# Performance work log

Hardware: AMD Instinct MI355X
Metric: run time of the kernel (lower is better)

Reference implementation:

```python
import jax, jax.numpy as jnp
import numpy as np
from jax.scipy.linalg import expm

HIDDEN = 1024
STATE = 64
INTER = 4096
EPS = 1e-06
DT_MIN, DT_MAX = 0.001, 0.1


def rmsnorm(x, w, eps=EPS):
    var = jnp.mean(x * x, axis=-1, keepdims=True)
    return x * jax.lax.rsqrt(var + eps) * w


def setup_inputs() -> dict:
    key = jax.random.key(0)
    ks = jax.random.split(key, 10)
    hidden_states = jax.random.normal(ks[0], (4, 2048, HIDDEN), dtype=jnp.float32)
    A = jax.random.normal(ks[1], (STATE, STATE), dtype=jnp.float32) * 0.01
    B = jax.random.normal(ks[2], (STATE, HIDDEN), dtype=jnp.float32) * 0.01
    C = jax.random.normal(ks[3], (HIDDEN, STATE), dtype=jnp.float32) * 0.01
    D = jnp.ones((HIDDEN,), dtype=jnp.float32)
    log_dt = jax.random.uniform(ks[4], (HIDDEN,), dtype=jnp.float32) * (np.log(DT_MAX) - np.log(DT_MIN)) + np.log(DT_MIN)
    s = 1.0 / np.sqrt(HIDDEN)
    w_gate = jax.random.uniform(ks[5], (INTER, HIDDEN), minval=-s, maxval=s, dtype=jnp.float32)
    w_up = jax.random.uniform(ks[6], (INTER, HIDDEN), minval=-s, maxval=s, dtype=jnp.float32)
    s2 = 1.0 / np.sqrt(INTER)
    w_down = jax.random.uniform(ks[7], (HIDDEN, INTER), minval=-s2, maxval=s2, dtype=jnp.float32)
    ln1_w = jnp.ones((HIDDEN,), dtype=jnp.float32)
    ln2_w = jnp.ones((HIDDEN,), dtype=jnp.float32)
    return {"hidden_states": hidden_states, "A": A, "B": B, "C": C, "D": D,
            "log_dt": log_dt, "w_gate": w_gate, "w_up": w_up, "w_down": w_down,
            "ln1_w": ln1_w, "ln2_w": ln2_w}


def ssm(x, A, B, C, D, log_dt):
    # x: (batch, seq, hidden)
    dt = jnp.exp(log_dt)                    # (hidden,)
    A_bar = expm(A * jnp.mean(dt))          # (state, state)
    B_bar = B * dt[None, :]                 # (state, hidden)

    def step(state, x_t):
        # state: (batch, state); x_t: (batch, hidden)
        state = state @ A_bar.T + x_t @ B_bar.T
        out = state @ C.T + D * x_t
        return state, out

    x_t = jnp.swapaxes(x, 0, 1)             # (seq, batch, hidden)
    init = jnp.zeros((x.shape[0], A.shape[0]), dtype=x.dtype)
    _, ys = jax.lax.scan(step, init, x_t)
    return jnp.swapaxes(ys, 0, 1)           # (batch, seq, hidden)


def reference(hidden_states, A, B, C, D, log_dt, w_gate, w_up, w_down, ln1_w, ln2_w):
    # pre-norm SSM mixer + residual
    residual = hidden_states
    h = rmsnorm(hidden_states, ln1_w)
    h = ssm(h, A, B, C, D, log_dt)
    h = residual + h
    # pre-norm SwiGLU FFN + residual
    residual = h
    hn = rmsnorm(h, ln2_w)
    gate = hn @ w_gate.T
    up = hn @ w_up.T
    ffn = (jax.nn.silu(gate) * up) @ w_down.T
    return residual + ffn
```

## Files before the change

### kernel.cpp

```cpp
#include <hip/hip_runtime.h>
#include <hip/hip_bf16.h>
#include <math.h>

typedef __attribute__((ext_vector_type(8))) short short8;
typedef __attribute__((ext_vector_type(4))) float f32x4;
typedef __attribute__((ext_vector_type(4))) int int4v;
typedef __attribute__((ext_vector_type(8))) int int8v;

__device__ __forceinline__ unsigned short f2b(float x) {
  union { float f; unsigned int u; } v; v.f = x;
  unsigned int r = v.u + 0x7fffu + ((v.u >> 16) & 1u);
  return (unsigned short)(r >> 16);
}
__device__ __forceinline__ float b2f(unsigned short u) {
  union { unsigned int u; float f; } v; v.u = ((unsigned int)u) << 16;
  return v.f;
}
__device__ __forceinline__ unsigned char f2f8_sw(float x) {
  float a = fabsf(x);
  unsigned char s = (x < 0.f) ? 0x80 : 0x00;
  if (a >= 464.f) return s | 0x7E;
  union { float f; unsigned u; } v; v.f = a;
  int e = (int)(v.u >> 23) - 127;
  if (e < -6) {
    int q = (int)rintf(a * 512.f);
    if (q >= 8) return s | 0x08;
    return s | (unsigned char)q;
  }
  unsigned mant = v.u & 0x7FFFFF;
  unsigned keep = mant >> 20;
  unsigned rest = mant & 0xFFFFF;
  if (rest > 0x80000u || (rest == 0x80000u && (keep & 1))) keep++;
  unsigned exp8 = (unsigned)(e + 7);
  if (keep == 8) { keep = 0; exp8++; }
  if (exp8 >= 15 && keep >= 7) return s | 0x7E;
  return s | (unsigned char)((exp8 << 3) | keep);
}
#if __has_builtin(__builtin_amdgcn_cvt_pk_fp8_f32)
__device__ __forceinline__ unsigned char f2f8(float x) {
  return (unsigned char)(__builtin_amdgcn_cvt_pk_fp8_f32(x, x, 0, false) & 0xFF);
}
__device__ __forceinline__ unsigned int f8pack4(float a, float b, float c, float d) {
  int w0 = __builtin_amdgcn_cvt_pk_fp8_f32(a, b, 0, false);
  return (unsigned int)__builtin_amdgcn_cvt_pk_fp8_f32(c, d, w0, true);
}
#else
__device__ __forceinline__ unsigned char f2f8(float x) { return f2f8_sw(x); }
__device__ __forceinline__ unsigned int f8pack4(float a, float b, float c, float d) {
  return (unsigned)f2f8_sw(a) | ((unsigned)f2f8_sw(b) << 8) |
         ((unsigned)f2f8_sw(c) << 16) | ((unsigned)f2f8_sw(d) << 24);
}
#endif
__device__ __forceinline__ void async_ld16(const void* g, void* l) {
  __builtin_amdgcn_global_load_lds(
      (const __attribute__((address_space(1))) void*)g,
      (__attribute__((address_space(3))) void*)l, 16, 0, 0);
}

#define VMCNT6()  asm volatile("s_waitcnt vmcnt(6)" ::: "memory")
#define VMCNT0()  asm volatile("s_waitcnt vmcnt(0)" ::: "memory")
#define LGKM0()   asm volatile("s_waitcnt lgkmcnt(0)" ::: "memory")

__device__ __forceinline__ f32x4 mx8(int8v a, int8v b, f32x4 c) {
#if __has_builtin(__builtin_amdgcn_mfma_scale_f32_16x16x128_f8f6f4)
  return __builtin_amdgcn_mfma_scale_f32_16x16x128_f8f6f4(
      a, b, c, 0, 0, 0, 0x7F7F7F7F, 0, 0x7F7F7F7F);
#else
  union { int8v v; long l[4]; } av, bv; av.v = a; bv.v = b;
#pragma unroll
  for (int j = 0; j < 4; j++)
    c = __builtin_amdgcn_mfma_f32_16x16x32_fp8_fp8(av.l[j], bv.l[j], c, 0, 0, 0);
  return c;
#endif
}

__global__ __launch_bounds__(1024) void prep_combo(
    const float* __restrict__ A, const float* __restrict__ logdt,
    float* __restrict__ Abar, float* __restrict__ A64,
    const float* __restrict__ B, const float* __restrict__ Cm,
    unsigned short* __restrict__ Bb, unsigned short* __restrict__ Cb) {
  __shared__ float red[16];
  __shared__ float Ms[4096], T[4096], P[4096];
  if (blockIdx.x != 0) {
    const size_t NB = 65536, NC = 65536;
    size_t base = (size_t)(blockIdx.x - 1) * 1024 + threadIdx.x;
    size_t stride = (size_t)(gridDim.x - 1) * 1024;
    for (size_t id = base; id < NB + NC; id += stride) {
      if (id < NB) { int k = (int)(id & 1023); Bb[id] = f2b(B[id] * expf(logdt[k])); }
      else Cb[id - NB] = f2b(Cm[id - NB]);
    }
    return;
  }
  const int tid = threadIdx.x;
  const int c = tid & 63;
  const int w = tid >> 6;
  float e = expf(logdt[tid]);
#pragma unroll
  for (int off = 32; off > 0; off >>= 1) e += __shfl_down(e, off);
  if (c == 0) red[w] = e;
  __syncthreads();
  if (tid == 0) {
    float s = 0.f;
    for (int i = 0; i < 16; i++) s += red[i];
    red[0] = s * (1.f / 1024.f);
  }
  __syncthreads();
  const float mdt = red[0];
  {
    float m0 = A[tid] * mdt, m1 = A[tid + 1024] * mdt,
          m2 = A[tid + 2048] * mdt, m3 = A[tid + 3072] * mdt;
    Ms[tid] = m0; Ms[tid + 1024] = m1; Ms[tid + 2048] = m2; Ms[tid + 3072] = m3;
    T[tid] = m0; T[tid + 1024] = m1; T[tid + 2048] = m2; T[tid + 3072] = m3;
    P[tid] = m0 + ((tid >> 6) == (tid & 63) ? 1.f : 0.f);
    P[tid + 1024] = m1 + (((tid + 1024) >> 6) == ((tid + 1024) & 63) ? 1.f : 0.f);
    P[tid + 2048] = m2 + (((tid + 2048) >> 6) == ((tid + 2048) & 63) ? 1.f : 0.f);
    P[tid + 3072] = m3 + (((tid + 3072) >> 6) == ((tid + 3072) & 63) ? 1.f : 0.f);
  }
  __syncthreads();
  float colM[64];
#pragma unroll
  for (int j = 0; j < 64; j++) colM[j] = Ms[j * 64 + c];
  for (int k = 2; k <= 6; k++) {
    const float inv = 1.f / (float)k;
    float accs[4];
#pragma unroll
    for (int i = 0; i < 4; i++) {
      const int r = w + 16 * i;
      const float4* Trow = (const float4*)(T + r * 64);
      float a0 = 0.f, a1 = 0.f, a2 = 0.f, a3 = 0.f;
#pragma unroll
      for (int j4 = 0; j4 < 16; j4++) {
        const float4 t = Trow[j4];
        a0 += t.x * colM[4 * j4 + 0]; a1 += t.y * colM[4 * j4 + 1];
        a2 += t.z * colM[4 * j4 + 2]; a3 += t.w * colM[4 * j4 + 3];
      }
      accs[i] = ((a0 + a1) + (a2 + a3)) * inv;
    }
    __syncthreads();
#pragma unroll
    for (int i = 0; i < 4; i++) {
      const int r = w + 16 * i;
      T[r * 64 + c] = accs[i];
      P[r * 64 + c] += accs[i];
    }
    __syncthreads();
  }
#pragma unroll
  for (int i = 0; i < 4; i++) {
    const int r = w + 16 * i;
    Abar[r * 64 + c] = P[r * 64 + c];
    T[r * 64 + c] = P[r * 64 + c];
  }
  __syncthreads();
  for (int sq = 0; sq < 6; sq++) {
    float colT[64];
#pragma unroll
    for (int j = 0; j < 64; j++) colT[j] = T[j * 64 + c];
    float accs[4];
#pragma unroll
    for (int i = 0; i < 4; i++) {
      const int r = w + 16 * i;
      const float4* Trow = (const float4*)(T + r * 64);
      float a0 = 0.f, a1 = 0.f, a2 = 0.f, a3 = 0.f;
#pragma unroll
      for (int j4 = 0; j4 < 16; j4++) {
        const float4 t = Trow[j4];
        a0 += t.x * colT[4 * j4 + 0]; a1 += t.y * colT[4 * j4 + 1];
        a2 += t.z * colT[4 * j4 + 2]; a3 += t.w * colT[4 * j4 + 3];
      }
      accs[i] = (a0 + a1) + (a2 + a3);
    }
    __syncthreads();
#pragma unroll
    for (int i = 0; i < 4; i++) T[(w + 16 * i) * 64 + c] = accs[i];
    __syncthreads();
  }
#pragma unroll
  for (int i = 0; i < 4; i++) {
    const int r = w + 16 * i;
    A64[r * 64 + c] = T[r * 64 + c];
  }
}

__global__ __launch_bounds__(256) void rmsnorm_bf16(
    const float* __restrict__ x, const float* __restrict__ w,
    unsigned short* __restrict__ out) {
  const size_t row = blockIdx.x;
  const int tid = threadIdx.x;
  const float4 v = ((const float4*)(x + row * 1024))[tid];
  float ss = v.x * v.x + v.y * v.y + v.z * v.z + v.w * v.w;
#pragma unroll
  for (int off = 32; off > 0; off >>= 1) ss += __shfl_down(ss, off);
  __shared__ float wsum[4];
  if ((tid & 63) == 0) wsum[tid >> 6] = ss;
  __syncthreads();
  const float tot = wsum[0] + wsum[1] + wsum[2] + wsum[3];
  const float rs = rsqrtf(tot * (1.f / 1024.f) + 1e-6f);
  const float4 wv = ((const float4*)w)[tid];
  ushort4 o;
  o.x = f2b(v.x * rs * wv.x); o.y = f2b(v.y * rs * wv.y);
  o.z = f2b(v.z * rs * wv.z); o.w = f2b(v.w * rs * wv.w);
  ((ushort4*)(out + row * 1024))[tid] = o;
}

__global__ __launch_bounds__(256) void rmsnorm_f8(
    const float* __restrict__ x, const float* __restrict__ w,
    unsigned int* __restrict__ out) {
  const size_t row = blockIdx.x;
  const int tid = threadIdx.x;
  const float4 v = ((const float4*)(x + row * 1024))[tid];
  float ss = v.x * v.x + v.y * v.y + v.z * v.z + v.w * v.w;
#pragma unroll
  for (int off = 32; off > 0; off >>= 1) ss += __shfl_down(ss, off);
  __shared__ float wsum[4];
  if ((tid & 63) == 0) wsum[tid >> 6] = ss;
  __syncthreads();
  const float tot = wsum[0] + wsum[1] + wsum[2] + wsum[3];
  const float rs = rsqrtf(tot * (1.f / 1024.f) + 1e-6f);
  const float4 wv = ((const float4*)w)[tid];
  out[row * 256 + tid] =
      f8pack4(v.x * rs * wv.x, v.y * rs * wv.y, v.z * rs * wv.z, v.w * rs * wv.w);
}

template <int STORE_S>
__global__ __launch_bounds__(256) void scan_combo(
    const float* __restrict__ U, const float* __restrict__ Abar,
    const float* __restrict__ carry, float* __restrict__ zend,
    unsigned short* __restrict__ S,
    const float* __restrict__ csrc, unsigned char* __restrict__ cdst, size_t ccount) {
  constexpr int SCAN_BLOCKS = 32;
  __shared__ float s[4][64];
  if (blockIdx.x >= SCAN_BLOCKS) {
    size_t base = (size_t)(blockIdx.x - SCAN_BLOCKS) * 256 + threadIdx.x;
    size_t stride = (size_t)(gridDim.x - SCAN_BLOCKS) * 256;
    for (size_t id = base; id < ccount; id += stride)
      cdst[id] = f2f8(csrc[id] * 64.f);
    return;
  }
  const int wave = threadIdx.x >> 6, i = threadIdx.x & 63;
  const int task = blockIdx.x * 4 + wave;
  const int b = task >> 5, c = task & 31;
  float a[64];
#pragma unroll
  for (int j = 0; j < 64; j++) a[j] = Abar[i * 64 + j];
  float cur = STORE_S ? carry[(b * 32 + c) * 64 + i] : 0.f;
  const float* Ub = U + ((size_t)(b * 2048 + c * 64)) * 64;
  for (int t = 0; t < 64; t++) {
    s[wave][i] = cur;
    __syncthreads();
    const float u = Ub[t * 64 + i];
    const float4* s4 = (const float4*)s[wave];
    float a0 = u, a1 = 0.f, a2 = 0.f, a3 = 0.f;
#pragma unroll
    for (int j = 0; j < 16; j++) {
      float4 v = s4[j];
      a0 += a[4 * j + 0] * v.x; a1 += a[4 * j + 1] * v.y;
      a2 += a[4 * j + 2] * v.z; a3 += a[4 * j + 3] * v.w;
    }
    cur = (a0 + a1) + (a2 + a3);
    __syncthreads();
    if (STORE_S) S[((size_t)(b * 2048 + c * 64 + t)) * 64 + i] = f2b(cur);
  }
  if (!STORE_S) zend[(b * 32 + c) * 64 + i] = cur;
}

__global__ __launch_bounds__(256) void carry_combo(
    const float* __restrict__ zend, const float* __restrict__ A64,
    float* __restrict__ carry,
    const float* __restrict__ csrc, unsigned char* __restrict__ cdst, size_t ccount) {
  __shared__ float s[4][64];
  if (blockIdx.x != 0) {
    size_t base = (size_t)(blockIdx.x - 1) * 256 + threadIdx.x;
    size_t stride = (size_t)(gridDim.x - 1) * 256;
    for (size_t id = base; id < ccount; id += stride)
      cdst[id] = f2f8(csrc[id] * 64.f);
    return;
  }
  const int b = threadIdx.x >> 6, i = threadIdx.x & 63;
  float a[64];
#pragma unroll
  for (int j = 0; j < 64; j++) a[j] = A64[i * 64 + j];
  float cur = 0.f;
  for (int c = 0; c < 32; c++) {
    carry[(b * 32 + c) * 64 + i] = cur;
    s[b][i] = cur;
    __syncthreads();
    const float z = zend[(b * 32 + c) * 64 + i];
    const float4* s4 = (const float4*)s[b];
    float a0 = z, a1 = 0.f, a2 = 0.f, a3 = 0.f;
#pragma unroll
    for (int j = 0; j < 16; j++) {
      float4 v = s4[j];
      a0 += a[4 * j + 0] * v.x; a1 += a[4 * j + 1] * v.y;
      a2 += a[4 * j + 2] * v.z; a3 += a[4 * j + 3] * v.w;
    }
    cur = (a0 + a1) + (a2 + a3);
    __syncthreads();
  }
}

template <int BM, int BN, int WAVES_M, int WAVES_N, int EPI>
__global__ void __launch_bounds__(256) gemm_bt(
    const unsigned short* __restrict__ X, const unsigned short* __restrict__ W,
    int M, int N, int K,
    float* __restrict__ outf, const unsigned short* __restrict__ e_b,
    const float* __restrict__ e_f, const float* __restrict__ e_d) {
  constexpr int BK = 64;
  constexpr int SM = BM / WAVES_M, SN = BN / WAVES_N;
  constexpr int TM = SM / 16, TN = SN / 16;
  __shared__ unsigned short aT[BM * BK];
  __shared__ unsigned short bT[BN * BK];
  const int tid = threadIdx.x;
  const int lane = tid & 63, wave = tid >> 6;
  const int wm = wave / WAVES_N, wn = wave % WAVES_N;
  const int lm = lane & 15, quad = lane >> 4;
  const long bm0 = (long)blockIdx.y * BM;
  const long bn0 = (long)blockIdx.x * BN;
  const int wb = tid & ~63;

  f32x4 acc[TM][TN];
#pragma unroll
  for (int i = 0; i < TM; i++)
#pragma unroll
    for (int j = 0; j < TN; j++) acc[i][j] = (f32x4){0.f, 0.f, 0.f, 0.f};

  for (int k0 = 0; k0 < K; k0 += BK) {
#pragma unroll
    for (int it = 0; it < (BM * 8) / 256; ++it) {
      int slot = it * 256 + tid;
      int r = slot >> 3, cp = slot & 7, c = cp ^ (r & 7);
      async_ld16(X + (bm0 + r) * (long)K + k0 + c * 8, aT + (it * 256 + wb) * 8);
    }
#pragma unroll
    for (int it = 0; it < (BN * 8) / 256; ++it) {
      int slot = it * 256 + tid;
      int r = slot >> 3, cp = slot & 7, c = cp ^ (r & 7);
      async_ld16(W + (bn0 + r) * (long)K + k0 + c * 8, bT + (it * 256 + wb) * 8);
    }
    __syncthreads();
#pragma unroll
    for (int kk = 0; kk < BK; kk += 32) {
      const int cch = (kk >> 3) + quad;
      short8 af[TM], bf[TN];
#pragma unroll
      for (int i = 0; i < TM; i++) {
        int r = wm * SM + i * 16 + lm;
        af[i] = *(const short8*)(aT + (r * 8 + (cch ^ (r & 7))) * 8);
      }
#pragma unroll
      for (int j = 0; j < TN; j++) {
        int r = wn * SN + j * 16 + lm;
        bf[j] = *(const short8*)(bT + (r * 8 + (cch ^ (r & 7))) * 8);
      }
#pragma unroll
      for (int i = 0; i < TM; i++)
#pragma unroll
        for (int j = 0; j < TN; j++)
          acc[i][j] = __builtin_amdgcn_mfma_f32_16x16x32_bf16(af[i], bf[j], acc[i][j], 0, 0, 0);
    }
    __syncthreads();
  }
#pragma unroll
  for (int i = 0; i < TM; i++) {
#pragma unroll
    for (int j = 0; j < TN; j++) {
#pragma unroll
      for (int r = 0; r < 4; r++) {
        const long m = bm0 + wm * SM + i * 16 + quad * 4 + r;
        const long n = bn0 + wn * SN + j * 16 + lm;
        const long idx = m * N + n;
        const float v = acc[i][j][r];
        if (EPI == 0) outf[idx] = v;
        else if (EPI == 4) outf[idx] = v + e_d[n] * b2f(e_b[idx]) + e_f[idx];
      }
    }
  }
}


__global__ void __launch_bounds__(512, 2) gemm_gu2(
    const unsigned char* __restrict__ X, const unsigned char* __restrict__ Wg,
    const unsigned char* __restrict__ Wu, int M, int N, int K,
    unsigned char* __restrict__ out8, float inv) {
  extern __shared__ __align__(64) unsigned char smem[];
  const int tid = threadIdx.x;
  const int lane = tid & 63, wave = tid >> 6, wb = tid & ~63;
  const int wm = wave >> 1, wn = wave & 1;
  const int lm = lane & 15, quad = lane >> 4;
  const long bm0 = (long)blockIdx.y * 256;
  const long bn0 = (long)blockIdx.x * 64;
  const unsigned char* Xb = X + bm0 * (long)K;
  const unsigned char* Gb = Wg + bn0 * (long)K;
  const unsigned char* Ub = Wu + bn0 * (long)K;
  const int NT = K >> 7;

  f32x4 accg[4][2], accu[4][2];
#pragma unroll
  for (int i = 0; i < 4; i++)
#pragma unroll
    for (int j = 0; j < 2; j++) {
      accg[i][j] = (f32x4){0.f, 0.f, 0.f, 0.f};
      accu[i][j] = (f32x4){0.f, 0.f, 0.f, 0.f};
    }

  auto stage = [&](int buf, int t) {
    unsigned char* base = smem + (size_t)buf * 49152;
    const long k0 = (long)t << 7;
#pragma unroll
    for (int it = 0; it < 4; ++it) {
      int slot = it * 512 + tid;
      int r = slot >> 3, cp = slot & 7;
      int cg = (((cp >> 1) ^ (r & 3)) << 1) | (cp & 1);
      async_ld16(Xb + (long)r * K + k0 + cg * 16, base + (size_t)(it * 512 + wb) * 16);
    }
    {
      int r = tid >> 3, cp = tid & 7;
      int cg = (((cp >> 1) ^ (r & 3)) << 1) | (cp & 1);
      async_ld16(Gb + (long)r * K + k0 + cg * 16, base + 32768 + (size_t)wb * 16);
      async_ld16(Ub + (long)r * K + k0 + cg * 16, base + 40960 + (size_t)wb * 16);
    }
  };
  auto compute = [&](int buf) {
    const unsigned char* base = smem + (size_t)buf * 49152;
    int8v a[4], g[2], u[2];
#pragma unroll
    for (int i = 0; i < 4; ++i) {
      int r = wm * 64 + i * 16 + lm;
      a[i] = *(const int8v*)(base + (size_t)((r << 2) + (quad ^ (r & 3))) * 32);
    }
#pragma unroll
    for (int j = 0; j < 2; ++j) {
      int r = wn * 32 + j * 16 + lm;
      size_t off = (size_t)((r << 2) + (quad ^ (r & 3))) * 32;
      g[j] = *(const int8v*)(base + 32768 + off);
      u[j] = *(const int8v*)(base + 40960 + off);
    }
    __builtin_amdgcn_s_setprio(1);
#pragma unroll
    for (int i = 0; i < 4; ++i)
#pragma unroll
      for (int j = 0; j < 2; ++j) {
        accg[i][j] = mx8(a[i], g[j], accg[i][j]);
        accu[i][j] = mx8(a[i], u[j], accu[i][j]);
      }
    __builtin_amdgcn_s_setprio(0);
  };

  stage(0, 0);
  stage(1, 1);
  VMCNT6();
  __builtin_amdgcn_s_barrier();
  int bcur = 0;
  for (int t = 0; t < NT; ++t) {
    if (t + 2 < NT) {
      const int bnext = (bcur + 2 >= 3) ? bcur - 1 : bcur + 2;
      stage(bnext, t + 2);
    }
    compute(bcur);
    if (t + 1 < NT) {
      LGKM0();
      if (t + 2 < NT) VMCNT6();
      else            VMCNT0();
      __builtin_amdgcn_s_barrier();
    }
    bcur = (bcur + 1 == 3) ? 0 : bcur + 1;
  }
#pragma unroll
  for (int i = 0; i < 4; i++) {
#pragma unroll
    for (int j = 0; j < 2; j++) {
#pragma unroll
      for (int r = 0; r < 4; r++) {
        const long m = bm0 + wm * 64 + i * 16 + quad * 4 + r;
        const long n = bn0 + wn * 32 + j * 16 + lm;
        const float gg = accg[i][j][r] * inv;
        const float uu = accu[i][j][r] * inv;
        const float s = gg / (1.f + __expf(-gg));
        out8[m * N + n] = f2f8(s * uu);
      }
    }
  }
}

__global__ void __launch_bounds__(512, 2) gemm_f82(
    const unsigned char* __restrict__ X, const unsigned char* __restrict__ W,
    int M, int N, int K,
    float* __restrict__ outf, const float* __restrict__ e_f, float inv) {
  extern __shared__ __align__(64) unsigned char smem[];
  const int tid = threadIdx.x;
  const int lane = tid & 63, wave = tid >> 6, wb = tid & ~63;
  const int wm = wave >> 1, wn = wave & 1;
  const int lm = lane & 15, quad = lane >> 4;
  const long bm0 = (long)blockIdx.y * 256;
  const long bn0 = (long)blockIdx.x * 128;
  const unsigned char* Xb = X + bm0 * (long)K;
  const unsigned char* Wb = W + bn0 * (long)K;
  const int NT = K >> 7;

  f32x4 acc[4][4];
#pragma unroll
  for (int i = 0; i < 4; i++)
#pragma unroll
    for (int j = 0; j < 4; j++) acc[i][j] = (f32x4){0.f, 0.f, 0.f, 0.f};

  auto stage = [&](int buf, int t) {
    unsigned char* base = smem + (size_t)buf * 49152;
    const long k0 = (long)t << 7;
#pragma unroll
    for (int it = 0; it < 4; ++it) {
      int slot = it * 512 + tid;
      int r = slot >> 3, cp = slot & 7;
      int cg = (((cp >> 1) ^ (r & 3)) << 1) | (cp & 1);
      async_ld16(Xb + (long)r * K + k0 + cg * 16, base + (size_t)(it * 512 + wb) * 16);
    }
#pragma unroll
    for (int it = 0; it < 2; ++it) {
      int slot = it * 512 + tid;
      int r = slot >> 3, cp = slot & 7;
      int cg = (((cp >> 1) ^ (r & 3)) << 1) | (cp & 1);
      async_ld16(Wb + (long)r * K + k0 + cg * 16, base + 32768 + (size_t)(it * 512 + wb) * 16);
    }
  };
  auto compute = [&](int buf) {
    const unsigned char* base = smem + (size_t)buf * 49152;
    int8v a[4], b[4];
#pragma unroll
    for (int i = 0; i < 4; ++i) {
      int r = wm * 64 + i * 16 + lm;
      a[i] = *(const int8v*)(base + (size_t)((r << 2) + (quad ^ (r & 3))) * 32);
    }
#pragma unroll
    for (int j = 0; j < 4; ++j) {
      int r = wn * 64 + j * 16 + lm;
      b[j] = *(const int8v*)(base + 32768 + (size_t)((r << 2) + (quad ^ (r & 3))) * 32);
    }
    __builtin_amdgcn_s_setprio(1);
#pragma unroll
    for (int i = 0; i < 4; ++i)
#pragma unroll
      for (int j = 0; j < 4; ++j)
        acc[i][j] = mx8(a[i], b[j], acc[i][j]);
    __builtin_amdgcn_s_setprio(0);
  };

  stage(0, 0);
  stage(1, 1);
  VMCNT6();
  __builtin_amdgcn_s_barrier();
  int bcur = 0;
  for (int t = 0; t < NT; ++t) {
    if (t + 2 < NT) {
      const int bnext = (bcur + 2 >= 3) ? bcur - 1 : bcur + 2;
      stage(bnext, t + 2);
    }
    compute(bcur);
    if (t + 1 < NT) {
      LGKM0();
      if (t + 2 < NT) VMCNT6();
      else            VMCNT0();
      __builtin_amdgcn_s_barrier();
    }
    bcur = (bcur + 1 == 3) ? 0 : bcur + 1;
  }
#pragma unroll
  for (int i = 0; i < 4; i++) {
#pragma unroll
    for (int j = 0; j < 4; j++) {
#pragma unroll
      for (int r = 0; r < 4; r++) {
        const long m = bm0 + wm * 64 + i * 16 + quad * 4 + r;
        const long n = bn0 + wn * 64 + j * 16 + lm;
        const long idx = m * N + n;
        outf[idx] = acc[i][j][r] * inv + e_f[idx];
      }
    }
  }
}

extern "C" void kernel_launch(void* const* d_in, const int* in_sizes, int n_in,
                              void* d_out, int out_size, void* d_ws, size_t ws_size,
                              hipStream_t stream) {
  const float* x     = (const float*)d_in[0];
  const float* A     = (const float*)d_in[1];
  const float* B     = (const float*)d_in[2];
  const float* C     = (const float*)d_in[3];
  const float* D     = (const float*)d_in[4];
  const float* logdt = (const float*)d_in[5];
  const float* wg    = (const float*)d_in[6];
  const float* wu    = (const float*)d_in[7];
  const float* wd    = (const float*)d_in[8];
  const float* ln1   = (const float*)d_in[9];
  const float* ln2   = (const float*)d_in[10];
  float* out = (float*)d_out;

  char* p = (char*)d_ws;
  auto alloc = [&](size_t bytes) { char* q = p; p += (bytes + 255) & ~(size_t)255; return q; };
  float* Abar  = (float*)alloc(64 * 64 * 4);
  float* A64   = (float*)alloc(64 * 64 * 4);
  float* zend  = (float*)alloc(4 * 32 * 64 * 4);
  float* carry = (float*)alloc(4 * 32 * 64 * 4);
  float* U     = (float*)alloc((size_t)8192 * 64 * 4);
  unsigned short* S    = (unsigned short*)alloc((size_t)8192 * 64 * 2);
  unsigned short* Bb   = (unsigned short*)alloc((size_t)64 * 1024 * 2);
  unsigned short* Cb   = (unsigned short*)alloc((size_t)1024 * 64 * 2);
  unsigned char*  wg8  = (unsigned char*)alloc((size_t)4096 * 1024);
  unsigned char*  wu8  = (unsigned char*)alloc((size_t)4096 * 1024);
  unsigned char*  wd8  = (unsigned char*)alloc((size_t)1024 * 4096);
  unsigned short* xnb  = (unsigned short*)alloc((size_t)8192 * 1024 * 2);
  unsigned char*  hn8  = (unsigned char*)alloc((size_t)8192 * 1024);
  float* h             = (float*)alloc((size_t)8192 * 1024 * 4);
  unsigned char*  act8 = (unsigned char*)alloc((size_t)8192 * 4096);

  const size_t NWG = (size_t)4096 * 1024;
  constexpr int DYN_LDS = 3 * 49152;

  static int lds_attr_done = 0;
  if (!lds_attr_done) {
    (void)hipFuncSetAttribute((const void*)gemm_gu2,
                              hipFuncAttributeMaxDynamicSharedMemorySize, DYN_LDS);
    (void)hipFuncSetAttribute((const void*)gemm_f82,
                              hipFuncAttributeMaxDynamicSharedMemorySize, DYN_LDS);
    lds_attr_done = 1;
  }

  prep_combo<<<33, 1024, 0, stream>>>(A, logdt, Abar, A64, B, C, Bb, Cb);
  rmsnorm_bf16<<<8192, 256, 0, stream>>>(x, ln1, xnb);
  gemm_bt<32, 64, 2, 2, 0><<<dim3(1, 256), 256, 0, stream>>>(
      xnb, Bb, 8192, 64, 1024, U, nullptr, nullptr, nullptr);
  scan_combo<0><<<32 + 1024, 256, 0, stream>>>(
      U, Abar, nullptr, zend, S, wg, wg8, NWG);
  carry_combo<<<1 + 1024, 256, 0, stream>>>(zend, A64, carry, wu, wu8, NWG);
  scan_combo<1><<<32 + 1024, 256, 0, stream>>>(
      U, Abar, carry, zend, S, wd, wd8, NWG);
  gemm_bt<128, 128, 2, 2, 4><<<dim3(8, 64), 256, 0, stream>>>(
      S, Cb, 8192, 1024, 64, h, xnb, x, D);
  rmsnorm_f8<<<8192, 256, 0, stream>>>(h, ln2, (unsigned int*)hn8);
  gemm_gu2<<<dim3(64, 32), 512, DYN_LDS, stream>>>(
      hn8, wg8, wu8, 8192, 4096, 1024, act8, 1.f / 64.f);
  gemm_f82<<<dim3(8, 32), 512, DYN_LDS, stream>>>(
      act8, wd8, 8192, 1024, 4096, out, h, 1.f / 64.f);
}
```

Before: 447.8 us.

## Shrink FP8 FFN GEMM tiles to 256 threads with double-buffered static LDS

Both FFN GEMMs now use 256-thread blocks with 128-row tiles (the down GEMM also halves its column tile). Triple-buffered dynamic LDS is replaced by double-buffered static shared memory with a full vmcnt(0) wait each k-step. This raises block count and occupancy, especially for the down projection, which previously launched few blocks. The cost is lower operand reuse per load and less latency hiding from the shallower pipeline.

```diff
diff --git a/kernel.cpp b/kernel.cpp
--- a/kernel.cpp
+++ b/kernel.cpp
@@ -57,7 +57,6 @@
       (__attribute__((address_space(3))) void*)l, 16, 0, 0);
 }
 
-#define VMCNT6()  asm volatile("s_waitcnt vmcnt(6)" ::: "memory")
 #define VMCNT0()  asm volatile("s_waitcnt vmcnt(0)" ::: "memory")
 #define LGKM0()   asm volatile("s_waitcnt lgkmcnt(0)" ::: "memory")
 
@@ -378,16 +377,17 @@
 }
 
 
-__global__ void __launch_bounds__(512, 2) gemm_gu2(
+__global__ void __launch_bounds__(256, 2) gemm_gu3(
     const unsigned char* __restrict__ X, const unsigned char* __restrict__ Wg,
     const unsigned char* __restrict__ Wu, int M, int N, int K,
     unsigned char* __restrict__ out8, float inv) {
-  extern __shared__ __align__(64) unsigned char smem[];
+  constexpr int BUF = 32768;
+  __shared__ __attribute__((aligned(64))) unsigned char smem[2 * BUF];
   const int tid = threadIdx.x;
   const int lane = tid & 63, wave = tid >> 6, wb = tid & ~63;
   const int wm = wave >> 1, wn = wave & 1;
   const int lm = lane & 15, quad = lane >> 4;
-  const long bm0 = (long)blockIdx.y * 256;
+  const long bm0 = (long)blockIdx.y * 128;
   const long bn0 = (long)blockIdx.x * 64;
   const unsigned char* Xb = X + bm0 * (long)K;
   const unsigned char* Gb = Wg + bn0 * (long)K;
@@ -404,24 +404,26 @@
     }
 
   auto stage = [&](int buf, int t) {
-    unsigned char* base = smem + (size_t)buf * 49152;
+    unsigned char* base = smem + buf * BUF;
     const long k0 = (long)t << 7;
 #pragma unroll
     for (int it = 0; it < 4; ++it) {
-      int slot = it * 512 + tid;
+      int slot = it * 256 + tid;
       int r = slot >> 3, cp = slot & 7;
       int cg = (((cp >> 1) ^ (r & 3)) << 1) | (cp & 1);
-      async_ld16(Xb + (long)r * K + k0 + cg * 16, base + (size_t)(it * 512 + wb) * 16);
-    }
-    {
-      int r = tid >> 3, cp = tid & 7;
+      async_ld16(Xb + (long)r * K + k0 + cg * 16, base + (it * 256 + wb) * 16);
+    }
+#pragma unroll
+    for (int it = 0; it < 2; ++it) {
+      int slot = it * 256 + tid;
+      int r = slot >> 3, cp = slot & 7;
       int cg = (((cp >> 1) ^ (r & 3)) << 1) | (cp & 1);
-      async_ld16(Gb + (long)r * K + k0 + cg * 16, base + 32768 + (size_t)wb * 16);
-      async_ld16(Ub + (long)r * K + k0 + cg * 16, base + 40960 + (size_t)wb * 16);
+      async_ld16(Gb + (long)r * K + k0 + cg * 16, base + 16384 + (it * 256 + wb) * 16);
+      async_ld16(Ub + (long)r * K + k0 + cg * 16, base + 24576 + (it * 256 + wb) * 16);
     }
   };
   auto compute = [&](int buf) {
-    const unsigned char* base = smem + (size_t)buf * 49152;
+    const unsigned char* base = smem + buf * BUF;
     int8v a[4], g[2], u[2];
 #pragma unroll
     for (int i = 0; i < 4; ++i) {
@@ -432,8 +434,8 @@
     for (int j = 0; j < 2; ++j) {
       int r = wn * 32 + j * 16 + lm;
       size_t off = (size_t)((r << 2) + (quad ^ (r & 3))) * 32;
-      g[j] = *(const int8v*)(base + 32768 + off);
-      u[j] = *(const int8v*)(base + 40960 + off);
+      g[j] = *(const int8v*)(base + 16384 + off);
+      u[j] = *(const int8v*)(base + 24576 + off);
     }
     __builtin_amdgcn_s_setprio(1);
 #pragma unroll
@@ -447,23 +449,18 @@
   };
 
   stage(0, 0);
-  stage(1, 1);
-  VMCNT6();
+  VMCNT0();
   __builtin_amdgcn_s_barrier();
-  int bcur = 0;
+  int cur = 0;
   for (int t = 0; t < NT; ++t) {
-    if (t + 2 < NT) {
-      const int bnext = (bcur + 2 >= 3) ? bcur - 1 : bcur + 2;
-      stage(bnext, t + 2);
-    }
-    compute(bcur);
+    if (t + 1 < NT) stage(cur ^ 1, t + 1);
+    compute(cur);
     if (t + 1 < NT) {
       LGKM0();
-      if (t + 2 < NT) VMCNT6();
-      else            VMCNT0();
+      VMCNT0();
       __builtin_amdgcn_s_barrier();
     }
-    bcur = (bcur + 1 == 3) ? 0 : bcur + 1;
+    cur ^= 1;
   }
 #pragma unroll
   for (int i = 0; i < 4; i++) {
@@ -482,94 +479,90 @@
   }
 }
 
-__global__ void __launch_bounds__(512, 2) gemm_f82(
+__global__ void __launch_bounds__(256, 2) gemm_f83(
     const unsigned char* __restrict__ X, const unsigned char* __restrict__ W,
     int M, int N, int K,
     float* __restrict__ outf, const float* __restrict__ e_f, float inv) {
-  extern __shared__ __align__(64) unsigned char smem[];
+  constexpr int BUF = 24576;
+  __shared__ __attribute__((aligned(64))) unsigned char smem[2 * BUF];
   const int tid = threadIdx.x;
   const int lane = tid & 63, wave = tid >> 6, wb = tid & ~63;
   const int wm = wave >> 1, wn = wave & 1;
   const int lm = lane & 15, quad = lane >> 4;
-  const long bm0 = (long)blockIdx.y * 256;
-  const long bn0 = (long)blockIdx.x * 128;
+  const long bm0 = (long)blockIdx.y * 128;
+  const long bn0 = (long)blockIdx.x * 64;
   const unsigned char* Xb = X + bm0 * (long)K;
   const unsigned char* Wb = W + bn0 * (long)K;
   const int NT = K >> 7;
 
-  f32x4 acc[4][4];
+  f32x4 acc[4][2];
 #pragma unroll
   for (int i = 0; i < 4; i++)
 #pragma unroll
-    for (int j = 0; j < 4; j++) acc[i][j] = (f32x4){0.f, 0.f, 0.f, 0.f};
+    for (int j = 0; j < 2; j++) acc[i][j] = (f32x4){0.f, 0.f, 0.f, 0.f};
 
   auto stage = [&](int buf, int t) {
-    unsigned char* base = smem + (size_t)buf * 49152;
+    unsigned char* base = smem + buf * BUF;
     const long k0 = (long)t << 7;
 #pragma unroll
     for (int it = 0; it < 4; ++it) {
-      int slot = it * 512 + tid;
+      int slot = it * 256 + tid;
       int r = slot >> 3, cp = slot & 7;
       int cg = (((cp >> 1) ^ (r & 3)) << 1) | (cp & 1);
-      async_ld16(Xb + (long)r * K + k0 + cg * 16, base + (size_t)(it * 512 + wb) * 16);
+      async_ld16(Xb + (long)r * K + k0 + cg * 16, base + (it * 256 + wb) * 16);
     }
 #pragma unroll
     for (int it = 0; it < 2; ++it) {
-      int slot = it * 512 + tid;
+      int slot = it * 256 + tid;
       int r = slot >> 3, cp = slot & 7;
       int cg = (((cp >> 1) ^ (r & 3)) << 1) | (cp & 1);
-      async_ld16(Wb + (long)r * K + k0 + cg * 16, base + 32768 + (size_t)(it * 512 + wb) * 16);
+      async_ld16(Wb + (long)r * K + k0 + cg * 16, base + 16384 + (it * 256 + wb) * 16);
     }
   };
   auto compute = [&](int buf) {
-    const unsigned char* base = smem + (size_t)buf * 49152;
-    int8v a[4], b[4];
+    const unsigned char* base = smem + buf * BUF;
+    int8v a[4], b[2];
 #pragma unroll
     for (int i = 0; i < 4; ++i) {
       int r = wm * 64 + i * 16 + lm;
       a[i] = *(const int8v*)(base + (size_t)((r << 2) + (quad ^ (r & 3))) * 32);
     }
 #pragma unroll
-    for (int j = 0; j < 4; ++j) {
-      int r = wn * 64 + j * 16 + lm;
-      b[j] = *(const int8v*)(base + 32768 + (size_t)((r << 2) + (quad ^ (r & 3))) * 32);
+    for (int j = 0; j < 2; ++j) {
+      int r = wn * 32 + j * 16 + lm;
+      b[j] = *(const int8v*)(base + 16384 + (size_t)((r << 2) + (quad ^ (r & 3))) * 32);
     }
     __builtin_amdgcn_s_setprio(1);
 #pragma unroll
     for (int i = 0; i < 4; ++i)
 #pragma unroll
-      for (int j = 0; j < 4; ++j)
+      for (int j = 0; j < 2; ++j)
         acc[i][j] = mx8(a[i], b[j], acc[i][j]);
     __builtin_amdgcn_s_setprio(0);
   };
 
   stage(0, 0);
-  stage(1, 1);
-  VMCNT6();
+  VMCNT0();
   __builtin_amdgcn_s_barrier();
-  int bcur = 0;
+  int cur = 0;
   for (int t = 0; t < NT; ++t) {
-    if (t + 2 < NT) {
-      const int bnext = (bcur + 2 >= 3) ? bcur - 1 : bcur + 2;
-      stage(bnext, t + 2);
-    }
-    compute(bcur);
+    if (t + 1 < NT) stage(cur ^ 1, t + 1);
+    compute(cur);
     if (t + 1 < NT) {
       LGKM0();
-      if (t + 2 < NT) VMCNT6();
-      else            VMCNT0();
+      VMCNT0();
       __builtin_amdgcn_s_barrier();
     }
-    bcur = (bcur + 1 == 3) ? 0 : bcur + 1;
+    cur ^= 1;
   }
 #pragma unroll
   for (int i = 0; i < 4; i++) {
 #pragma unroll
-    for (int j = 0; j < 4; j++) {
+    for (int j = 0; j < 2; j++) {
 #pragma unroll
       for (int r = 0; r < 4; r++) {
         const long m = bm0 + wm * 64 + i * 16 + quad * 4 + r;
-        const long n = bn0 + wn * 64 + j * 16 + lm;
+        const long n = bn0 + wn * 32 + j * 16 + lm;
         const long idx = m * N + n;
         outf[idx] = acc[i][j][r] * inv + e_f[idx];
       }
@@ -612,16 +605,6 @@
   unsigned char*  act8 = (unsigned char*)alloc((size_t)8192 * 4096);
 
   const size_t NWG = (size_t)4096 * 1024;
-  constexpr int DYN_LDS = 3 * 49152;
-
-  static int lds_attr_done = 0;
-  if (!lds_attr_done) {
-    (void)hipFuncSetAttribute((const void*)gemm_gu2,
-                              hipFuncAttributeMaxDynamicSharedMemorySize, DYN_LDS);
-    (void)hipFuncSetAttribute((const void*)gemm_f82,
-                              hipFuncAttributeMaxDynamicSharedMemorySize, DYN_LDS);
-    lds_attr_done = 1;
-  }
 
   prep_combo<<<33, 1024, 0, stream>>>(A, logdt, Abar, A64, B, C, Bb, Cb);
   rmsnorm_bf16<<<8192, 256, 0, stream>>>(x, ln1, xnb);
@@ -635,8 +618,8 @@
   gemm_bt<128, 128, 2, 2, 4><<<dim3(8, 64), 256, 0, stream>>>(
       S, Cb, 8192, 1024, 64, h, xnb, x, D);
   rmsnorm_f8<<<8192, 256, 0, stream>>>(h, ln2, (unsigned int*)hn8);
-  gemm_gu2<<<dim3(64, 32), 512, DYN_LDS, stream>>>(
+  gemm_gu3<<<dim3(64, 64), 256, 0, stream>>>(
       hn8, wg8, wu8, 8192, 4096, 1024, act8, 1.f / 64.f);
-  gemm_f82<<<dim3(8, 32), 512, DYN_LDS, stream>>>(
+  gemm_f83<<<dim3(16, 64), 256, 0, stream>>>(
       act8, wd8, 8192, 1024, 4096, out, h, 1.f / 64.f);
 }
```

Result: no change. 442.6 us (-1.2%).

## Interleave FP8 GEMM staging with per-row-block MFMA phases and 8-way LDS swizzle

Applied to the files above, without the earlier changes.

Both FP8 GEMMs (gate/up and down) now split each K-tile iteration into four phases. Each phase issues one A-fragment LDS read and a slice of the next-next tile's async global-to-LDS loads, then runs its MFMAs between barriers. The LDS swizzle changes from a 4-way XOR on 32-byte chunks to an 8-way XOR on 16-byte chunks, read as two 16-byte halves, to cut bank conflicts. The intent is to overlap global loads, LDS reads and matrix ops more finely. In exchange it adds several workgroup barriers per tile and drops the explicit lgkmcnt wait.

```diff
diff --git a/kernel.cpp b/kernel.cpp
--- a/kernel.cpp
+++ b/kernel.cpp
@@ -59,7 +59,6 @@
 
 #define VMCNT6()  asm volatile("s_waitcnt vmcnt(6)" ::: "memory")
 #define VMCNT0()  asm volatile("s_waitcnt vmcnt(0)" ::: "memory")
-#define LGKM0()   asm volatile("s_waitcnt lgkmcnt(0)" ::: "memory")
 
 __device__ __forceinline__ f32x4 mx8(int8v a, int8v b, f32x4 c) {
 #if __has_builtin(__builtin_amdgcn_mfma_scale_f32_16x16x128_f8f6f4)
@@ -72,6 +71,13 @@
     c = __builtin_amdgcn_mfma_f32_16x16x32_fp8_fp8(av.l[j], bv.l[j], c, 0, 0, 0);
   return c;
 #endif
+}
+
+__device__ __forceinline__ int8v rd8(const unsigned char* tb, int r, int q) {
+  union { int8v v; int4v h[2]; } x;
+  x.h[0] = *(const int4v*)(tb + (size_t)((r << 3) + ((2 * q)     ^ (r & 7))) * 16);
+  x.h[1] = *(const int4v*)(tb + (size_t)((r << 3) + ((2 * q + 1) ^ (r & 7))) * 16);
+  return x.v;
 }
 
 __global__ __launch_bounds__(1024) void prep_combo(
@@ -378,10 +384,11 @@
 }
 
 
-__global__ void __launch_bounds__(512, 2) gemm_gu2(
+__global__ void __launch_bounds__(512, 2) gemm_gu4(
     const unsigned char* __restrict__ X, const unsigned char* __restrict__ Wg,
     const unsigned char* __restrict__ Wu, int M, int N, int K,
     unsigned char* __restrict__ out8, float inv) {
+  constexpr int BUF = 49152;
   extern __shared__ __align__(64) unsigned char smem[];
   const int tid = threadIdx.x;
   const int lane = tid & 63, wave = tid >> 6, wb = tid & ~63;
@@ -403,67 +410,67 @@
       accu[i][j] = (f32x4){0.f, 0.f, 0.f, 0.f};
     }
 
-  auto stage = [&](int buf, int t) {
-    unsigned char* base = smem + (size_t)buf * 49152;
-    const long k0 = (long)t << 7;
-#pragma unroll
-    for (int it = 0; it < 4; ++it) {
-      int slot = it * 512 + tid;
-      int r = slot >> 3, cp = slot & 7;
-      int cg = (((cp >> 1) ^ (r & 3)) << 1) | (cp & 1);
-      async_ld16(Xb + (long)r * K + k0 + cg * 16, base + (size_t)(it * 512 + wb) * 16);
-    }
-    {
-      int r = tid >> 3, cp = tid & 7;
-      int cg = (((cp >> 1) ^ (r & 3)) << 1) | (cp & 1);
-      async_ld16(Gb + (long)r * K + k0 + cg * 16, base + 32768 + (size_t)wb * 16);
-      async_ld16(Ub + (long)r * K + k0 + cg * 16, base + 40960 + (size_t)wb * 16);
-    }
+  auto stA = [&](unsigned char* base, int t, int it) {
+    int slot = it * 512 + tid;
+    int r = slot >> 3, cp = slot & 7, c = cp ^ (r & 7);
+    async_ld16(Xb + (long)r * K + ((long)t << 7) + c * 16,
+               base + (size_t)(it * 512 + wb) * 16);
   };
-  auto compute = [&](int buf) {
-    const unsigned char* base = smem + (size_t)buf * 49152;
-    int8v a[4], g[2], u[2];
-#pragma unroll
-    for (int i = 0; i < 4; ++i) {
-      int r = wm * 64 + i * 16 + lm;
-      a[i] = *(const int8v*)(base + (size_t)((r << 2) + (quad ^ (r & 3))) * 32);
-    }
-#pragma unroll
-    for (int j = 0; j < 2; ++j) {
-      int r = wn * 32 + j * 16 + lm;
-      size_t off = (size_t)((r << 2) + (quad ^ (r & 3))) * 32;
-      g[j] = *(const int8v*)(base + 32768 + off);
-      u[j] = *(const int8v*)(base + 40960 + off);
-    }
-    __builtin_amdgcn_s_setprio(1);
-#pragma unroll
-    for (int i = 0; i < 4; ++i)
-#pragma unroll
-      for (int j = 0; j < 2; ++j) {
-        accg[i][j] = mx8(a[i], g[j], accg[i][j]);
-        accu[i][j] = mx8(a[i], u[j], accu[i][j]);
-      }
-    __builtin_amdgcn_s_setprio(0);
+  auto stG = [&](unsigned char* base, int t) {
+    int r = tid >> 3, cp = tid & 7, c = cp ^ (r & 7);
+    async_ld16(Gb + (long)r * K + ((long)t << 7) + c * 16,
+               base + 32768 + (size_t)wb * 16);
   };
-
-  stage(0, 0);
-  stage(1, 1);
+  auto stU = [&](unsigned char* base, int t) {
+    int r = tid >> 3, cp = tid & 7, c = cp ^ (r & 7);
+    async_ld16(Ub + (long)r * K + ((long)t << 7) + c * 16,
+               base + 40960 + (size_t)wb * 16);
+  };
+  auto stage_all = [&](unsigned char* base, int t) {
+    stA(base, t, 0); stA(base, t, 1); stA(base, t, 2); stA(base, t, 3);
+    stG(base, t);    stU(base, t);
+  };
+
+  stage_all(smem, 0);
+  stage_all(smem + BUF, 1);
   VMCNT6();
   __builtin_amdgcn_s_barrier();
-  int bcur = 0;
+
   for (int t = 0; t < NT; ++t) {
-    if (t + 2 < NT) {
-      const int bnext = (bcur + 2 >= 3) ? bcur - 1 : bcur + 2;
-      stage(bnext, t + 2);
-    }
-    compute(bcur);
+    const unsigned char* cur = smem + (size_t)(t % 3) * BUF;
+    const unsigned char* bG = cur + 32768;
+    const unsigned char* bU = cur + 40960;
+    const int st = t + 2;
+    unsigned char* sb = smem + (size_t)(st % 3) * BUF;
+    int8v gf[2], uf[2];
+#pragma unroll
+    for (int p = 0; p < 4; ++p) {
+      int8v ap = rd8(cur, wm * 64 + p * 16 + lm, quad);
+      if (p == 0) {
+        gf[0] = rd8(bG, wn * 32 + lm, quad);
+        gf[1] = rd8(bG, wn * 32 + 16 + lm, quad);
+        uf[0] = rd8(bU, wn * 32 + lm, quad);
+        uf[1] = rd8(bU, wn * 32 + 16 + lm, quad);
+      }
+      if (st < NT) {
+        if (p == 0)      { stA(sb, st, 0); stA(sb, st, 1); }
+        else if (p == 1) { stA(sb, st, 2); stA(sb, st, 3); }
+        else if (p == 2) { stG(sb, st);    stU(sb, st); }
+      }
+      __builtin_amdgcn_s_barrier();
+      __builtin_amdgcn_s_setprio(1);
+      accg[p][0] = mx8(ap, gf[0], accg[p][0]);
+      accg[p][1] = mx8(ap, gf[1], accg[p][1]);
+      accu[p][0] = mx8(ap, uf[0], accu[p][0]);
+      accu[p][1] = mx8(ap, uf[1], accu[p][1]);
+      __builtin_amdgcn_s_setprio(0);
+      if (p < 3) __builtin_amdgcn_s_barrier();
+    }
     if (t + 1 < NT) {
-      LGKM0();
-      if (t + 2 < NT) VMCNT6();
-      else            VMCNT0();
+      if (st < NT) VMCNT6();
+      else         VMCNT0();
       __builtin_amdgcn_s_barrier();
     }
-    bcur = (bcur + 1 == 3) ? 0 : bcur + 1;
   }
 #pragma unroll
   for (int i = 0; i < 4; i++) {
@@ -482,10 +489,11 @@
   }
 }
 
-__global__ void __launch_bounds__(512, 2) gemm_f82(
+__global__ void __launch_bounds__(512, 2) gemm_f84(
     const unsigned char* __restrict__ X, const unsigned char* __restrict__ W,
     int M, int N, int K,
     float* __restrict__ outf, const float* __restrict__ e_f, float inv) {
+  constexpr int BUF = 49152;
   extern __shared__ __align__(64) unsigned char smem[];
   const int tid = threadIdx.x;
   const int lane = tid & 63, wave = tid >> 6, wb = tid & ~63;
@@ -503,64 +511,62 @@
 #pragma unroll
     for (int j = 0; j < 4; j++) acc[i][j] = (f32x4){0.f, 0.f, 0.f, 0.f};
 
-  auto stage = [&](int buf, int t) {
-    unsigned char* base = smem + (size_t)buf * 49152;
-    const long k0 = (long)t << 7;
-#pragma unroll
-    for (int it = 0; it < 4; ++it) {
-      int slot = it * 512 + tid;
-      int r = slot >> 3, cp = slot & 7;
-      int cg = (((cp >> 1) ^ (r & 3)) << 1) | (cp & 1);
-      async_ld16(Xb + (long)r * K + k0 + cg * 16, base + (size_t)(it * 512 + wb) * 16);
-    }
-#pragma unroll
-    for (int it = 0; it < 2; ++it) {
-      int slot = it * 512 + tid;
-      int r = slot >> 3, cp = slot & 7;
-      int cg = (((cp >> 1) ^ (r & 3)) << 1) | (cp & 1);
-      async_ld16(Wb + (long)r * K + k0 + cg * 16, base + 32768 + (size_t)(it * 512 + wb) * 16);
-    }
+  auto stA = [&](unsigned char* base, int t, int it) {
+    int slot = it * 512 + tid;
+    int r = slot >> 3, cp = slot & 7, c = cp ^ (r & 7);
+    async_ld16(Xb + (long)r * K + ((long)t << 7) + c * 16,
+               base + (size_t)(it * 512 + wb) * 16);
   };
-  auto compute = [&](int buf) {
-    const unsigned char* base = smem + (size_t)buf * 49152;
-    int8v a[4], b[4];
-#pragma unroll
-    for (int i = 0; i < 4; ++i) {
-      int r = wm * 64 + i * 16 + lm;
-      a[i] = *(const int8v*)(base + (size_t)((r << 2) + (quad ^ (r & 3))) * 32);
-    }
-#pragma unroll
-    for (int j = 0; j < 4; ++j) {
-      int r = wn * 64 + j * 16 + lm;
-      b[j] = *(const int8v*)(base + 32768 + (size_t)((r << 2) + (quad ^ (r & 3))) * 32);
-    }
-    __builtin_amdgcn_s_setprio(1);
-#pragma unroll
-    for (int i = 0; i < 4; ++i)
-#pragma unroll
-      for (int j = 0; j < 4; ++j)
-        acc[i][j] = mx8(a[i], b[j], acc[i][j]);
-    __builtin_amdgcn_s_setprio(0);
+  auto stB = [&](unsigned char* base, int t, int it) {
+    int slot = it * 512 + tid;
+    int r = slot >> 3, cp = slot & 7, c = cp ^ (r & 7);
+    async_ld16(Wb + (long)r * K + ((long)t << 7) + c * 16,
+               base + 32768 + (size_t)(it * 512 + wb) * 16);
   };
-
-  stage(0, 0);
-  stage(1, 1);
+  auto stage_all = [&](unsigned char* base, int t) {
+    stA(base, t, 0); stA(base, t, 1); stA(base, t, 2); stA(base, t, 3);
+    stB(base, t, 0); stB(base, t, 1);
+  };
+
+  stage_all(smem, 0);
+  stage_all(smem + BUF, 1);
   VMCNT6();
   __builtin_amdgcn_s_barrier();
-  int bcur = 0;
+
   for (int t = 0; t < NT; ++t) {
-    if (t + 2 < NT) {
-      const int bnext = (bcur + 2 >= 3) ? bcur - 1 : bcur + 2;
-      stage(bnext, t + 2);
-    }
-    compute(bcur);
+    const unsigned char* cur = smem + (size_t)(t % 3) * BUF;
+    const unsigned char* bB = cur + 32768;
+    const int st = t + 2;
+    unsigned char* sb = smem + (size_t)(st % 3) * BUF;
+    int8v bf[4];
+#pragma unroll
+    for (int p = 0; p < 4; ++p) {
+      int8v ap = rd8(cur, wm * 64 + p * 16 + lm, quad);
+      if (p == 0) {
+        bf[0] = rd8(bB, wn * 64 + lm, quad);
+        bf[1] = rd8(bB, wn * 64 + 16 + lm, quad);
+        bf[2] = rd8(bB, wn * 64 + 32 + lm, quad);
+        bf[3] = rd8(bB, wn * 64 + 48 + lm, quad);
+      }
+      if (st < NT) {
+        if (p == 0)      { stA(sb, st, 0); stA(sb, st, 1); }
+        else if (p == 1) { stA(sb, st, 2); stA(sb, st, 3); }
+        else if (p == 2) { stB(sb, st, 0); stB(sb, st, 1); }
+      }
+      __builtin_amdgcn_s_barrier();
+      __builtin_amdgcn_s_setprio(1);
+      acc[p][0] = mx8(ap, bf[0], acc[p][0]);
+      acc[p][1] = mx8(ap, bf[1], acc[p][1]);
+      acc[p][2] = mx8(ap, bf[2], acc[p][2]);
+      acc[p][3] = mx8(ap, bf[3], acc[p][3]);
+      __builtin_amdgcn_s_setprio(0);
+      if (p < 3) __builtin_amdgcn_s_barrier();
+    }
     if (t + 1 < NT) {
-      LGKM0();
-      if (t + 2 < NT) VMCNT6();
-      else            VMCNT0();
+      if (st < NT) VMCNT6();
+      else         VMCNT0();
       __builtin_amdgcn_s_barrier();
     }
-    bcur = (bcur + 1 == 3) ? 0 : bcur + 1;
   }
 #pragma unroll
   for (int i = 0; i < 4; i++) {
@@ -616,9 +622,9 @@
 
   static int lds_attr_done = 0;
   if (!lds_attr_done) {
-    (void)hipFuncSetAttribute((const void*)gemm_gu2,
+    (void)hipFuncSetAttribute((const void*)gemm_gu4,
                               hipFuncAttributeMaxDynamicSharedMemorySize, DYN_LDS);
-    (void)hipFuncSetAttribute((const void*)gemm_f82,
+    (void)hipFuncSetAttribute((const void*)gemm_f84,
                               hipFuncAttributeMaxDynamicSharedMemorySize, DYN_LDS);
     lds_attr_done = 1;
   }
@@ -635,8 +641,8 @@
   gemm_bt<128, 128, 2, 2, 4><<<dim3(8, 64), 256, 0, stream>>>(
       S, Cb, 8192, 1024, 64, h, xnb, x, D);
   rmsnorm_f8<<<8192, 256, 0, stream>>>(h, ln2, (unsigned int*)hn8);
-  gemm_gu2<<<dim3(64, 32), 512, DYN_LDS, stream>>>(
+  gemm_gu4<<<dim3(64, 32), 512, DYN_LDS, stream>>>(
       hn8, wg8, wu8, 8192, 4096, 1024, act8, 1.f / 64.f);
-  gemm_f82<<<dim3(8, 32), 512, DYN_LDS, stream>>>(
+  gemm_f84<<<dim3(8, 32), 512, DYN_LDS, stream>>>(
       act8, wd8, 8192, 1024, 4096, out, h, 1.f / 64.f);
 }
```

Result: faster. 429.1 us (-4.2%).
